# Kernel optimization log

Hardware: AMD Instinct MI355X
Metric: run time of the kernel (lower is better)

The kernel has to match this reference:

```python
import jax, jax.numpy as jnp
import numpy as np

D = 128   # hidden_size
L = 50    # mailbox length (USER_MAX_LEN / ITEM_MAX_LEN)
NU = 8192 # num user nodes
NI = 8192 # num item nodes


def setup_inputs() -> dict:
    key = jax.random.key(0)
    ks = jax.random.split(key, 16)
    s = 0.05
    return {
        "user": jax.random.normal(ks[0], (NU, D), jnp.float32),
        "item": jax.random.normal(ks[1], (NI, D), jnp.float32),
        "W_user": jax.random.normal(ks[2], (D, D), jnp.float32) * s,
        "W_item": jax.random.normal(ks[3], (D, D), jnp.float32) * s,
        "agg_gate_user": jax.random.normal(ks[4], (2 * D, D), jnp.float32) * s,
        "agg_gate_item": jax.random.normal(ks[5], (2 * D, D), jnp.float32) * s,
        "update_user": jax.random.normal(ks[6], (2 * D, D), jnp.float32) * s,
        "update_item": jax.random.normal(ks[7], (2 * D, D), jnp.float32) * s,
        "user_date_emb": jax.random.normal(ks[8], (L, D), jnp.float32) * s,
        "user_date_emb_k": jax.random.normal(ks[9], (L, D), jnp.float32) * s,
        "item_date_emb": jax.random.normal(ks[10], (L, D), jnp.float32) * s,
        "item_date_emb_k": jax.random.normal(ks[11], (L, D), jnp.float32) * s,
        "user_nbr": jax.random.randint(ks[12], (NU, L), 0, NI, jnp.int64) if jax.config.jax_enable_x64 else jax.random.randint(ks[12], (NU, L), 0, NI, jnp.int32),
        "user_nbr_time": jax.random.randint(ks[13], (NU, L), 0, 1000000, jnp.int32),
        "item_nbr": jax.random.randint(ks[14], (NI, L), 0, NU, jnp.int32),
        "item_nbr_time": jax.random.randint(ks[15], (NI, L), 0, 1000000, jnp.int32),
    }


def _reduce(dst_h, src_mail, time, emb, emb_k, gate_W):
    # dst_h: [N,d], src_mail: [N,L,d], time: [N,L]
    # double argsort -> rank; reorder = L - rank - 1 (time-order position)
    order = jnp.argsort(jnp.argsort(time, axis=1), axis=1)
    reorder = time.shape[1] - order - 1                     # [N,L]
    scale = 1.0 / jnp.sqrt(jnp.asarray(dst_h.shape[-1], dst_h.dtype))
    # long-term attention with positional injection
    e = jnp.sum((emb[reorder] + src_mail) * dst_h[:, None, :], axis=-1) * scale
    alpha = jax.nn.softmax(e, axis=1)                       # [N,L]
    h_long = jnp.einsum('nl,nld->nd', alpha, src_mail + emb_k[reorder])
    # short-term attention against most-recent neighbor
    last = jnp.argmax(time, axis=1)                         # [N]
    last_emb = jnp.take_along_axis(src_mail, last[:, None, None], axis=1)  # [N,1,d]
    e1 = jnp.sum(last_emb * src_mail, axis=-1) * scale
    alpha1 = jax.nn.softmax(e1, axis=1)
    h_short = jnp.einsum('nl,nld->nd', alpha1, src_mail)
    return jnp.concatenate([h_long, h_short], axis=-1) @ gate_W  # [N,d]


def reference(user, item, W_user, W_item, agg_gate_user, agg_gate_item,
              update_user, update_item, user_date_emb, user_date_emb_k,
              item_date_emb, item_date_emb_k, user_nbr, user_nbr_time,
              item_nbr, item_nbr_time):
    # feat_drop/attn_drop are identity (eval mode)
    uh = user @ W_user   # [NU,d]
    ih = item @ W_item   # [NI,d]
    # user nodes aggregate item-neighbor mailboxes
    user_agg = _reduce(uh, ih[user_nbr], user_nbr_time,
                       user_date_emb, user_date_emb_k, agg_gate_user)
    # item nodes aggregate user-neighbor mailboxes
    item_agg = _reduce(ih, uh[item_nbr], item_nbr_time,
                       item_date_emb, item_date_emb_k, agg_gate_item)
    user_out = jnp.tanh(jnp.concatenate([user_agg, user], axis=-1) @ update_user)
    item_out = jnp.tanh(jnp.concatenate([item_agg, item], axis=-1) @ update_item)
    return user_out, item_out
```

## Files before the change

### kernel.cpp

```cpp
#include <hip/hip_runtime.h>
#include <math.h>

#define D 128
#define L 50
#define SCALE 0.08838834764831845f

using bf16x8 = __attribute__((ext_vector_type(8))) short;
using f32x4  = __attribute__((ext_vector_type(4))) float;

union FragU { bf16x8 f; uint2 u2[2]; uint4 u4; };

__device__ __forceinline__ unsigned f2bf(float x) {
    union { float f; unsigned u; } v; v.f = x;
    return (v.u + 0x7fffu + ((v.u >> 16) & 1u)) >> 16;
}
__device__ __forceinline__ float bflo(unsigned u) {
    union { unsigned u; float f; } v; v.u = u << 16; return v.f;
}
__device__ __forceinline__ float bfhi(unsigned u) {
    union { unsigned u; float f; } v; v.u = u & 0xffff0000u; return v.f;
}

__global__ __launch_bounds__(256) void prep_all_kernel(
    const float* __restrict__ Wu, const float* __restrict__ Wi,
    const float* __restrict__ ue, const float* __restrict__ ie,
    const float* __restrict__ gu, const float* __restrict__ gi,
    const float* __restrict__ uu, const float* __restrict__ ui,
    const float* __restrict__ uek, const float* __restrict__ iek,
    unsigned short* __restrict__ Bptu, unsigned short* __restrict__ Bpti,
    unsigned short* __restrict__ Btu, unsigned short* __restrict__ Bti)
{
    __shared__ float T[2][128];
    int b = blockIdx.x, t = threadIdx.x;
    if (b < 50) {
        int side = b / 25;
        int o = (b % 25) * 256 + t;
        int d = o / L, l = o % L;
        const float* W = side ? Wi : Wu;
        const float* E = side ? ie : ue;
        unsigned short* Bpt = side ? Bpti : Bptu;
        float a = 0.f;
        for (int k = 0; k < D; ++k) a += W[d * D + k] * E[l * D + k];
        Bpt[(128 + l) * 128 + d] = (unsigned short)f2bf(a);
    } else if (b < 306) {
        int bb = b - 50;
        int side = bb / 128;
        int o = (bb % 128) * 256 + t;
        int r = o >> 7, c = o & 127;
        const float* G = side ? gi : gu;
        const float* U = side ? ui : uu;
        unsigned short* Bt = side ? Bti : Btu;
        float a = 0.f;
        for (int k = 0; k < D; ++k) a += G[r * D + k] * U[k * D + c];
        Bt[c * 448 + r] = (unsigned short)f2bf(a);
    } else if (b < 434) {
        int bb = b - 306;
        int side = bb >> 6;
        int o = (bb & 63) * 256 + t;
        int r = o >> 7, c = o & 127;
        const float* U = side ? ui : uu;
        unsigned short* Bt = side ? Bti : Btu;
        Bt[c * 448 + 320 + r] = (unsigned short)f2bf(U[(128 + r) * D + c]);
        if (r < 14) Bt[c * 448 + 306 + r] = 0;
    } else if (b < 562) {
        int bb = b - 434;
        int side = bb >> 6;
        int o = (bb & 63) * 256 + t;
        int k = o >> 7, c = o & 127;
        const float* W = side ? Wi : Wu;
        unsigned short* Bpt = side ? Bpti : Bptu;
        Bpt[c * 128 + k] = (unsigned short)f2bf(W[k * D + c]);
    } else if (b < 564) {
        int side = b - 562;
        unsigned short* Bpt = side ? Bpti : Bptu;
        for (int j = 0; j < 7; ++j)
            Bpt[178 * 128 + t * 7 + j] = 0;
    } else {
        int bb = b - 564;
        int side = bb / 25;
        int ro = (bb % 25) * 2;
        const float* EK = side ? iek : uek;
        const float* G  = side ? gi : gu;
        const float* U  = side ? ui : uu;
        unsigned short* Bt = side ? Bti : Btu;
        int r = t >> 7, c = t & 127;
        float a = 0.f;
        for (int k = 0; k < D; ++k) a += EK[(ro + r) * D + k] * G[k * D + c];
        T[r][c] = a;
        __syncthreads();
        float e = 0.f;
        for (int j = 0; j < D; ++j) e += T[r][j] * U[j * D + c];
        Bt[c * 448 + 256 + ro + r] = (unsigned short)f2bf(e);
    }
}

__global__ __launch_bounds__(256) void proj_mfma(
    const float* __restrict__ Xu, const float* __restrict__ Xi,
    const unsigned* __restrict__ Bptu32, const unsigned* __restrict__ Bpti32,
    unsigned* __restrict__ h32, float* __restrict__ eproj,
    unsigned* __restrict__ A32, int NU)
{
    __shared__ __align__(16) unsigned Bs[192 * 68];
    int t = threadIdx.x;
    int nb = blockIdx.x * 32;
    const float* X = (nb < NU) ? Xu : Xi;
    int xoff = (nb < NU) ? 0 : NU;
    const unsigned* Bt = (nb < NU) ? Bptu32 : Bpti32;
    int wave = t >> 6, lane = t & 63;
    int m16 = lane & 15, quad = lane >> 4;

    #pragma unroll
    for (int i = 0; i < 12; ++i) {
        int idx = t + i * 256;
        int c = idx >> 4, q = idx & 15;
        uint4 v = *(const uint4*)&Bt[(size_t)c * 64 + q * 4];
        *(uint4*)&Bs[c * 68 + q * 4] = v;
    }
    __syncthreads();

    f32x4 acc[2][3];
    for (int i = 0; i < 2; ++i)
        for (int j = 0; j < 3; ++j) acc[i][j] = (f32x4){0.f, 0.f, 0.f, 0.f};

    #pragma unroll
    for (int kc = 0; kc < 4; ++kc) {
        FragU a[2];
        #pragma unroll
        for (int mi = 0; mi < 2; ++mi) {
            int row = nb + mi * 16 + m16;
            const float* src = &X[(size_t)(row - xoff) * D + kc * 32 + quad * 8];
            float4 v0 = *(const float4*)&src[0];
            float4 v1 = *(const float4*)&src[4];
            uint4 pk;
            pk.x = f2bf(v0.x) | (f2bf(v0.y) << 16);
            pk.y = f2bf(v0.z) | (f2bf(v0.w) << 16);
            pk.z = f2bf(v1.x) | (f2bf(v1.y) << 16);
            pk.w = f2bf(v1.z) | (f2bf(v1.w) << 16);
            a[mi].u4 = pk;
            if (wave == 0)
                *(uint4*)&A32[(size_t)row * 224 + 160 + kc * 16 + quad * 4] = pk;
        }
        #pragma unroll
        for (int ni = 0; ni < 3; ++ni) {
            bf16x8 bb = *(const bf16x8*)&Bs[(wave * 48 + ni * 16 + m16) * 68 + kc * 16 + quad * 4];
            acc[0][ni] = __builtin_amdgcn_mfma_f32_16x16x32_bf16(a[0].f, bb, acc[0][ni], 0, 0, 0);
            acc[1][ni] = __builtin_amdgcn_mfma_f32_16x16x32_bf16(a[1].f, bb, acc[1][ni], 0, 0, 0);
        }
    }
    #pragma unroll
    for (int mi = 0; mi < 2; ++mi)
        #pragma unroll
        for (int ni = 0; ni < 3; ++ni) {
            int col = wave * 48 + ni * 16 + m16;
            #pragma unroll
            for (int r = 0; r < 4; ++r) {
                float me = acc[mi][ni][r];
                float pr = __shfl_xor(me, 1);
                int row = nb + mi * 16 + quad * 4 + r;
                if (col < 128) {
                    if (!(lane & 1))
                        h32[(size_t)row * 64 + (col >> 1)] = f2bf(me) | (f2bf(pr) << 16);
                } else if (col < 178) {
                    eproj[(size_t)row * L + (col - 128)] = me;
                }
            }
        }
}

__global__ __launch_bounds__(256) void agg_kernel(
    const unsigned* __restrict__ h32, const float* __restrict__ eproj,
    const int* __restrict__ unbr, const int* __restrict__ untime,
    const int* __restrict__ inbr, const int* __restrict__ intime,
    unsigned* __restrict__ A32, int NU, int NI)
{
    __shared__ unsigned smail[2][L * 66];
    __shared__ unsigned shb[2][64];
    __shared__ float se2[2][2][64];
    __shared__ float salpha[2][L], salpha1[2][L];
    __shared__ int stime[2][L], sreorder[2][L], snbr[2][L], slast[2];

    int tb = threadIdx.x;
    int sub = tb >> 7;
    int t = tb & 127;
    int g = blockIdx.x * 2 + sub;
    int wave = t >> 6, lane = t & 63;
    int m16 = lane & 15, quad = lane >> 4;

    const unsigned* mail; const int* nbrp; const int* timp;
    if (g < NU) { mail = h32 + (size_t)NU * 64; nbrp = unbr + (size_t)g * L;        timp = untime + (size_t)g * L; }
    else        { mail = h32;                   nbrp = inbr + (size_t)(g - NU) * L; timp = intime + (size_t)(g - NU) * L; }

    if (t < 64) shb[sub][t] = h32[(size_t)g * 64 + t];
    if (t < L) { stime[sub][t] = timp[t]; snbr[sub][t] = nbrp[t]; }
    __syncthreads();

    if (t < L) {
        int ti = stime[sub][t]; int rank = 0; bool firstmax = true;
        for (int j = 0; j < L; ++j) {
            int tj = stime[sub][j];
            rank += (tj < ti) || (tj == ti && j < t);
            firstmax = firstmax && ((tj < ti) || (tj == ti && j >= t));
        }
        sreorder[sub][t] = L - 1 - rank;
        if (firstmax) slast[sub] = t;
    }
    {
        int q = t >> 5, p = t & 31;
        #pragma unroll
        for (int i = 0; i < 13; ++i) {
            int l = i * 4 + q;
            if (l < L) {
                uint2 v = *(const uint2*)&mail[(size_t)snbr[sub][l] * 64 + p * 2];
                *(uint2*)&smail[sub][l * 66 + 2 * p] = v;
            }
        }
    }
    __syncthreads();

    {
        const unsigned* bptr = (m16 == 1) ? &smail[sub][slast[sub] * 66]
                                          : &shb[sub][0];
        int s0 = wave * 32 + m16;  if (s0 > 49) s0 = 49;
        int s1 = wave * 32 + 16 + m16;  if (s1 > 49) s1 = 49;
        const unsigned* a0p = &smail[sub][s0 * 66];
        const unsigned* a1p = &smail[sub][s1 * 66];
        f32x4 d0 = {0.f, 0.f, 0.f, 0.f}, d1 = {0.f, 0.f, 0.f, 0.f};
        #pragma unroll
        for (int kc = 0; kc < 4; ++kc) {
            int off = kc * 16 + quad * 4;
            FragU bf_, af0, af1;
            bf_.u2[0] = *(const uint2*)&bptr[off];
            bf_.u2[1] = *(const uint2*)&bptr[off + 2];
            af0.u2[0] = *(const uint2*)&a0p[off];
            af0.u2[1] = *(const uint2*)&a0p[off + 2];
            af1.u2[0] = *(const uint2*)&a1p[off];
            af1.u2[1] = *(const uint2*)&a1p[off + 2];
            d0 = __builtin_amdgcn_mfma_f32_16x16x32_bf16(af0.f, bf_.f, d0, 0, 0, 0);
            d1 = __builtin_amdgcn_mfma_f32_16x16x32_bf16(af1.f, bf_.f, d1, 0, 0, 0);
        }
        if (m16 < 2) {
            #pragma unroll
            for (int r = 0; r < 4; ++r) {
                se2[sub][m16][wave * 32 + quad * 4 + r]      = d0[r];
                se2[sub][m16][wave * 32 + 16 + quad * 4 + r] = d1[r];
            }
        }
    }
    __syncthreads();

    float sc = -1e30f;
    if (lane < L) {
        sc = (wave == 0)
           ? (se2[sub][0][lane] + eproj[(size_t)g * L + sreorder[sub][lane]]) * SCALE
           : se2[sub][1][lane] * SCALE;
    }
    float mx = sc;
    for (int off = 32; off; off >>= 1) mx = fmaxf(mx, __shfl_xor(mx, off));
    float ex = (lane < L) ? expf(sc - mx) : 0.f;
    float sm = ex;
    for (int off = 32; off; off >>= 1) sm += __shfl_xor(sm, off);
    float al = ex / sm;
    if (lane < L) { if (wave == 0) salpha[sub][lane] = al; else salpha1[sub][lane] = al; }
    __syncthreads();

    {
        const float* alp = wave ? salpha1[sub] : salpha[sub];
        const unsigned* base = &smail[sub][lane];
        float ax = 0.f, ay = 0.f;
        for (int l = 0; l < L; ++l) {
            unsigned u = base[l * 66];
            float a = alp[l];
            ax += a * bflo(u);
            ay += a * bfhi(u);
        }
        A32[(size_t)g * 224 + wave * 64 + lane] = f2bf(ax) | (f2bf(ay) << 16);
    }
    if (t >= 64 && t < 96) A32[(size_t)g * 224 + 128 + (t - 64)] = 0u;
    __syncthreads();
    if (t < L) {
        ((unsigned short*)A32)[(size_t)g * 448 + 256 + sreorder[sub][t]] =
            (unsigned short)f2bf(salpha[sub][t]);
    }
}

__global__ __launch_bounds__(256) void gemm_out_mfma(
    const unsigned* __restrict__ A32,
    const unsigned* __restrict__ Btu32, const unsigned* __restrict__ Bti32,
    float* __restrict__ out, int NU)
{
    __shared__ __align__(16) unsigned Bs[64 * 228];
    int t = threadIdx.x;
    int rowblk = blockIdx.x >> 1, half = blockIdx.x & 1;
    int nb = rowblk * 128;
    const unsigned* Bt = (nb < NU) ? Btu32 : Bti32;
    int wave = t >> 6, lane = t & 63;
    int m16 = lane & 15, quad = lane >> 4;

    #pragma unroll
    for (int i = 0; i < 14; ++i) {
        int idx = t + i * 256;
        int n = idx / 56, q = idx - n * 56;
        uint4 v = *(const uint4*)&Bt[(size_t)(half * 64 + n) * 224 + q * 4];
        *(uint4*)&Bs[n * 228 + q * 4] = v;
    }
    __syncthreads();

    #pragma unroll
    for (int j = 0; j < 2; ++j) {
        int mrow0 = nb + (wave * 2 + j) * 16;
        f32x4 acc[4] = {{0.f,0.f,0.f,0.f},{0.f,0.f,0.f,0.f},
                        {0.f,0.f,0.f,0.f},{0.f,0.f,0.f,0.f}};
        for (int kc = 0; kc < 14; ++kc) {
            FragU af;
            af.u4 = *(const uint4*)&A32[(size_t)(mrow0 + m16) * 224 + kc * 16 + quad * 4];
            #pragma unroll
            for (int ni = 0; ni < 4; ++ni) {
                bf16x8 bf = *(const bf16x8*)&Bs[(ni * 16 + m16) * 228 + kc * 16 + quad * 4];
                acc[ni] = __builtin_amdgcn_mfma_f32_16x16x32_bf16(af.f, bf, acc[ni], 0, 0, 0);
            }
        }
        #pragma unroll
        for (int ni = 0; ni < 4; ++ni)
            #pragma unroll
            for (int r = 0; r < 4; ++r) {
                int row = mrow0 + quad * 4 + r;
                int col = half * 64 + ni * 16 + m16;
                out[(size_t)row * D + col] = tanhf(acc[ni][r]);
            }
    }
}

extern "C" void kernel_launch(void* const* d_in, const int* in_sizes, int n_in,
                              void* d_out, int out_size, void* d_ws, size_t ws_size,
                              hipStream_t stream) {
    const float* user   = (const float*)d_in[0];
    const float* item   = (const float*)d_in[1];
    const float* Wu     = (const float*)d_in[2];
    const float* Wi     = (const float*)d_in[3];
    const float* gate_u = (const float*)d_in[4];
    const float* gate_i = (const float*)d_in[5];
    const float* upd_u  = (const float*)d_in[6];
    const float* upd_i  = (const float*)d_in[7];
    const float* uemb   = (const float*)d_in[8];
    const float* uembk  = (const float*)d_in[9];
    const float* iemb   = (const float*)d_in[10];
    const float* iembk  = (const float*)d_in[11];
    const int*   unbr   = (const int*)d_in[12];
    const int*   untime = (const int*)d_in[13];
    const int*   inbr   = (const int*)d_in[14];
    const int*   intime = (const int*)d_in[15];

    int NU = in_sizes[0] / D;
    int NI = in_sizes[1] / D;
    int N  = NU + NI;

    float* eproj  = (float*)d_ws;
    unsigned* h32   = (unsigned*)(eproj + (size_t)N * L);
    unsigned* A32   = h32 + (size_t)N * 64;
    unsigned* Btu32 = A32 + (size_t)N * 224;
    unsigned* Bti32 = Btu32 + 128 * 224;
    unsigned* Bptu32 = Bti32 + 128 * 224;
    unsigned* Bpti32 = Bptu32 + 192 * 64;

    prep_all_kernel<<<614, 256, 0, stream>>>(Wu, Wi, uemb, iemb, gate_u, gate_i,
                                             upd_u, upd_i, uembk, iembk,
                                             (unsigned short*)Bptu32,
                                             (unsigned short*)Bpti32,
                                             (unsigned short*)Btu32,
                                             (unsigned short*)Bti32);
    proj_mfma<<<N / 32, 256, 0, stream>>>(user, item, Bptu32, Bpti32,
                                          h32, eproj, A32, NU);
    agg_kernel<<<N / 2, 256, 0, stream>>>(h32, eproj, unbr, untime, inbr,
                                          intime, A32, NU, NI);
    gemm_out_mfma<<<N / 64, 256, 0, stream>>>(A32, Btu32, Bti32,
                                              (float*)d_out, NU);
}
```

Measured before the change: 173.3 us.

## Restructure aggregation to one node per block with MFMA alpha-weighted sums

The aggregation kernel now handles one node per 256-thread block instead of two nodes per block. The mailbox is gathered with 16-byte loads into registers, stored row-major, and also stored transposed with an XOR swizzle. The alpha-weighted sums over the 50 neighbours move from a scalar FMA loop to bf16 MFMA against the transposed mailbox, with the alphas packed to bf16. The rank computation is unrolled with vector LDS reads. This trades more blocks and a heavier scatter-transpose into LDS, plus bf16 rounding of the alphas, for fewer serial FMA iterations and wider memory accesses.

```diff
diff --git a/kernel.cpp b/kernel.cpp
--- a/kernel.cpp
+++ b/kernel.cpp
@@ -173,114 +173,153 @@
     const int* __restrict__ inbr, const int* __restrict__ intime,
     unsigned* __restrict__ A32, int NU, int NI)
 {
-    __shared__ unsigned smail[2][L * 66];
-    __shared__ unsigned shb[2][64];
-    __shared__ float se2[2][2][64];
-    __shared__ float salpha[2][L], salpha1[2][L];
-    __shared__ int stime[2][L], sreorder[2][L], snbr[2][L], slast[2];
-
-    int tb = threadIdx.x;
-    int sub = tb >> 7;
-    int t = tb & 127;
-    int g = blockIdx.x * 2 + sub;
-    int wave = t >> 6, lane = t & 63;
+    __shared__ __align__(16) unsigned smrow[50 * 68];
+    __shared__ __align__(16) unsigned short sT[128 * 56 + 16];
+    __shared__ __align__(16) unsigned shb[64];
+    __shared__ __align__(16) unsigned salb[64];
+    __shared__ float se2[2][64];
+    __shared__ __align__(16) int stime[52];
+    __shared__ int sreorder[50], snbr[50], slast;
+
+    int t = threadIdx.x;
+    int g = blockIdx.x;
+    int wv = t >> 6, lane = t & 63;
     int m16 = lane & 15, quad = lane >> 4;
 
     const unsigned* mail; const int* nbrp; const int* timp;
     if (g < NU) { mail = h32 + (size_t)NU * 64; nbrp = unbr + (size_t)g * L;        timp = untime + (size_t)g * L; }
     else        { mail = h32;                   nbrp = inbr + (size_t)(g - NU) * L; timp = intime + (size_t)(g - NU) * L; }
 
-    if (t < 64) shb[sub][t] = h32[(size_t)g * 64 + t];
-    if (t < L) { stime[sub][t] = timp[t]; snbr[sub][t] = nbrp[t]; }
-    __syncthreads();
+    if (t < 64) shb[t] = h32[(size_t)g * 64 + t];
+    if (t < L) { stime[t] = timp[t]; snbr[t] = nbrp[t]; }
+    __syncthreads();
+
+    uint4 vbuf[4];
+    #pragma unroll
+    for (int p = 0; p < 4; ++p) {
+        int c = t + p * 256;
+        if (c < 800) {
+            int r = c >> 4, q = c & 15;
+            vbuf[p] = *(const uint4*)&mail[(size_t)snbr[r] * 64 + q * 4];
+        }
+    }
 
     if (t < L) {
-        int ti = stime[sub][t]; int rank = 0; bool firstmax = true;
-        for (int j = 0; j < L; ++j) {
-            int tj = stime[sub][j];
-            rank += (tj < ti) || (tj == ti && j < t);
-            firstmax = firstmax && ((tj < ti) || (tj == ti && j >= t));
-        }
-        sreorder[sub][t] = L - 1 - rank;
-        if (firstmax) slast[sub] = t;
-    }
+        int ti = stime[t];
+        int rank = 0, bad = 0;
+        #pragma unroll
+        for (int j4 = 0; j4 < 48; j4 += 4) {
+            int4 v = *(const int4*)&stime[j4];
+            int tj;
+            tj = v.x; rank += (tj < ti) || (tj == ti && (j4 + 0) < t); bad |= (tj > ti) || (tj == ti && (j4 + 0) < t);
+            tj = v.y; rank += (tj < ti) || (tj == ti && (j4 + 1) < t); bad |= (tj > ti) || (tj == ti && (j4 + 1) < t);
+            tj = v.z; rank += (tj < ti) || (tj == ti && (j4 + 2) < t); bad |= (tj > ti) || (tj == ti && (j4 + 2) < t);
+            tj = v.w; rank += (tj < ti) || (tj == ti && (j4 + 3) < t); bad |= (tj > ti) || (tj == ti && (j4 + 3) < t);
+        }
+        {
+            int2 v = *(const int2*)&stime[48];
+            int tj;
+            tj = v.x; rank += (tj < ti) || (tj == ti && 48 < t); bad |= (tj > ti) || (tj == ti && 48 < t);
+            tj = v.y; rank += (tj < ti) || (tj == ti && 49 < t); bad |= (tj > ti) || (tj == ti && 49 < t);
+        }
+        sreorder[t] = L - 1 - rank;
+        if (!bad) slast = t;
+    }
+
+    #pragma unroll
+    for (int p = 0; p < 4; ++p) {
+        int c = t + p * 256;
+        if (c < 800) {
+            int r = c >> 4, q = c & 15;
+            uint4 v = vbuf[p];
+            *(uint4*)&smrow[r * 68 + q * 4] = v;
+            int rowbase = q * 8, xq = q & 7;
+            sT[(rowbase + (0 ^ xq)) * 56 + r] = (unsigned short)(v.x & 0xffff);
+            sT[(rowbase + (1 ^ xq)) * 56 + r] = (unsigned short)(v.x >> 16);
+            sT[(rowbase + (2 ^ xq)) * 56 + r] = (unsigned short)(v.y & 0xffff);
+            sT[(rowbase + (3 ^ xq)) * 56 + r] = (unsigned short)(v.y >> 16);
+            sT[(rowbase + (4 ^ xq)) * 56 + r] = (unsigned short)(v.z & 0xffff);
+            sT[(rowbase + (5 ^ xq)) * 56 + r] = (unsigned short)(v.z >> 16);
+            sT[(rowbase + (6 ^ xq)) * 56 + r] = (unsigned short)(v.w & 0xffff);
+            sT[(rowbase + (7 ^ xq)) * 56 + r] = (unsigned short)(v.w >> 16);
+        }
+    }
+    if (t >= 144 && t < 240) {
+        int idx = t - 144;
+        int r = 50 + (idx >> 4), q = idx & 15;
+        #pragma unroll
+        for (int j = 0; j < 8; ++j) sT[(q * 8 + j) * 56 + r] = 0;
+    }
+    if (t < 16) sT[128 * 56 + t] = 0;
+    __syncthreads();
+
     {
-        int q = t >> 5, p = t & 31;
-        #pragma unroll
-        for (int i = 0; i < 13; ++i) {
-            int l = i * 4 + q;
-            if (l < L) {
-                uint2 v = *(const uint2*)&mail[(size_t)snbr[sub][l] * 64 + p * 2];
-                *(uint2*)&smail[sub][l * 66 + 2 * p] = v;
-            }
-        }
-    }
-    __syncthreads();
-
-    {
-        const unsigned* bptr = (m16 == 1) ? &smail[sub][slast[sub] * 66]
-                                          : &shb[sub][0];
-        int s0 = wave * 32 + m16;  if (s0 > 49) s0 = 49;
-        int s1 = wave * 32 + 16 + m16;  if (s1 > 49) s1 = 49;
-        const unsigned* a0p = &smail[sub][s0 * 66];
-        const unsigned* a1p = &smail[sub][s1 * 66];
-        f32x4 d0 = {0.f, 0.f, 0.f, 0.f}, d1 = {0.f, 0.f, 0.f, 0.f};
+        int s = wv * 16 + m16; if (s > 49) s = 49;
+        int last = slast;
+        f32x4 dd = {0.f, 0.f, 0.f, 0.f};
         #pragma unroll
         for (int kc = 0; kc < 4; ++kc) {
-            int off = kc * 16 + quad * 4;
-            FragU bf_, af0, af1;
-            bf_.u2[0] = *(const uint2*)&bptr[off];
-            bf_.u2[1] = *(const uint2*)&bptr[off + 2];
-            af0.u2[0] = *(const uint2*)&a0p[off];
-            af0.u2[1] = *(const uint2*)&a0p[off + 2];
-            af1.u2[0] = *(const uint2*)&a1p[off];
-            af1.u2[1] = *(const uint2*)&a1p[off + 2];
-            d0 = __builtin_amdgcn_mfma_f32_16x16x32_bf16(af0.f, bf_.f, d0, 0, 0, 0);
-            d1 = __builtin_amdgcn_mfma_f32_16x16x32_bf16(af1.f, bf_.f, d1, 0, 0, 0);
+            FragU af, bf_;
+            af.u4 = *(const uint4*)&smrow[s * 68 + kc * 16 + quad * 4];
+            if (m16 == 1) bf_.u4 = *(const uint4*)&smrow[last * 68 + kc * 16 + quad * 4];
+            else          bf_.u4 = *(const uint4*)&shb[kc * 16 + quad * 4];
+            dd = __builtin_amdgcn_mfma_f32_16x16x32_bf16(af.f, bf_.f, dd, 0, 0, 0);
         }
         if (m16 < 2) {
             #pragma unroll
-            for (int r = 0; r < 4; ++r) {
-                se2[sub][m16][wave * 32 + quad * 4 + r]      = d0[r];
-                se2[sub][m16][wave * 32 + 16 + quad * 4 + r] = d1[r];
+            for (int r = 0; r < 4; ++r)
+                se2[m16][wv * 16 + quad * 4 + r] = dd[r];
+        }
+    }
+    __syncthreads();
+
+    if (wv < 2) {
+        float sc = -1e30f;
+        if (lane < L) {
+            sc = (wv == 0)
+               ? (se2[0][lane] + eproj[(size_t)g * L + sreorder[lane]]) * SCALE
+               : se2[1][lane] * SCALE;
+        }
+        float mx = sc;
+        for (int off = 32; off; off >>= 1) mx = fmaxf(mx, __shfl_xor(mx, off));
+        float ex = (lane < L) ? expf(sc - mx) : 0.f;
+        float sm = ex;
+        for (int off = 32; off; off >>= 1) sm += __shfl_xor(sm, off);
+        float al = ex / sm;
+        float alo = __shfl_xor(al, 1);
+        if (!(lane & 1))
+            salb[wv * 32 + (lane >> 1)] = f2bf(al) | (f2bf(alo) << 16);
+    }
+    if (t >= 128 && t < 160) A32[(size_t)g * 224 + 128 + (t - 128)] = 0u;
+    __syncthreads();
+
+    {
+        FragU a0, a1;
+        int arow = (m16 & 1) * 32;
+        a0.u4 = *(const uint4*)&salb[arow + quad * 4];
+        a1.u4 = *(const uint4*)&salb[arow + 16 + quad * 4];
+        unsigned short* Au = (unsigned short*)A32 + (size_t)g * 448;
+        #pragma unroll
+        for (int ni = 0; ni < 2; ++ni) {
+            int dblk = wv * 2 + ni;
+            int d = dblk * 16 + m16;
+            int phys = d ^ ((d >> 3) & 7);
+            const unsigned short* rowp = &sT[phys * 56];
+            FragU fb0, fb1;
+            fb0.u4 = *(const uint4*)&rowp[quad * 8];
+            fb1.u4 = *(const uint4*)&rowp[32 + quad * 8];
+            f32x4 acc = {0.f, 0.f, 0.f, 0.f};
+            acc = __builtin_amdgcn_mfma_f32_16x16x32_bf16(a0.f, fb0.f, acc, 0, 0, 0);
+            acc = __builtin_amdgcn_mfma_f32_16x16x32_bf16(a1.f, fb1.f, acc, 0, 0, 0);
+            if (quad == 0) {
+                Au[dblk * 16 + m16]       = (unsigned short)f2bf(acc[0]);
+                Au[128 + dblk * 16 + m16] = (unsigned short)f2bf(acc[1]);
             }
         }
     }
-    __syncthreads();
-
-    float sc = -1e30f;
-    if (lane < L) {
-        sc = (wave == 0)
-           ? (se2[sub][0][lane] + eproj[(size_t)g * L + sreorder[sub][lane]]) * SCALE
-           : se2[sub][1][lane] * SCALE;
-    }
-    float mx = sc;
-    for (int off = 32; off; off >>= 1) mx = fmaxf(mx, __shfl_xor(mx, off));
-    float ex = (lane < L) ? expf(sc - mx) : 0.f;
-    float sm = ex;
-    for (int off = 32; off; off >>= 1) sm += __shfl_xor(sm, off);
-    float al = ex / sm;
-    if (lane < L) { if (wave == 0) salpha[sub][lane] = al; else salpha1[sub][lane] = al; }
-    __syncthreads();
-
-    {
-        const float* alp = wave ? salpha1[sub] : salpha[sub];
-        const unsigned* base = &smail[sub][lane];
-        float ax = 0.f, ay = 0.f;
-        for (int l = 0; l < L; ++l) {
-            unsigned u = base[l * 66];
-            float a = alp[l];
-            ax += a * bflo(u);
-            ay += a * bfhi(u);
-        }
-        A32[(size_t)g * 224 + wave * 64 + lane] = f2bf(ax) | (f2bf(ay) << 16);
-    }
-    if (t >= 64 && t < 96) A32[(size_t)g * 224 + 128 + (t - 64)] = 0u;
-    __syncthreads();
-    if (t < L) {
-        ((unsigned short*)A32)[(size_t)g * 448 + 256 + sreorder[sub][t]] =
-            (unsigned short)f2bf(salpha[sub][t]);
-    }
+    if (t < L)
+        ((unsigned short*)A32)[(size_t)g * 448 + 256 + sreorder[t]] =
+            ((const unsigned short*)&salb[0])[t];
 }
 
 __global__ __launch_bounds__(256) void gemm_out_mfma(
@@ -370,8 +409,8 @@
                                              (unsigned short*)Bti32);
     proj_mfma<<<N / 32, 256, 0, stream>>>(user, item, Bptu32, Bpti32,
                                           h32, eproj, A32, NU);
-    agg_kernel<<<N / 2, 256, 0, stream>>>(h32, eproj, unbr, untime, inbr,
-                                          intime, A32, NU, NI);
+    agg_kernel<<<N, 256, 0, stream>>>(h32, eproj, unbr, untime, inbr,
+                                      intime, A32, NU, NI);
     gemm_out_mfma<<<N / 64, 256, 0, stream>>>(A32, Btu32, Bti32,
                                               (float*)d_out, NU);
 }
```

New measurement: 191.8 us. 1.11x slower.
